# Kernel optimization log

Measured on AMD Instinct MI355X. Metric: run time of the kernel, lower is better.

The kernel has to match this reference:

```python
import jax, jax.numpy as jnp
import numpy as np

LRELU = 0.2
BN_EPS = 1e-5
SN_EPS = 1e-12


def _spectral_norm(w, u):
    # One power iteration (torch train-mode behavior), u/v detached.
    wm = w.reshape(w.shape[0], -1)            # [out, in*kh*kw]
    u = jax.lax.stop_gradient(u)
    v = wm.T @ u
    v = v / (jnp.linalg.norm(v) + SN_EPS)
    u2 = wm @ v
    u2 = u2 / (jnp.linalg.norm(u2) + SN_EPS)
    sigma = u2 @ (wm @ v)
    return w / sigma


def _conv(x, w):
    # Conv2d kernel=4, stride=2, padding=1, no bias
    return jax.lax.conv_general_dilated(
        x, w, window_strides=(2, 2), padding=((1, 1), (1, 1)),
        dimension_numbers=("NCHW", "OIHW", "NCHW"))


def _bn(x, g, b):
    # BatchNorm2d in training mode: biased batch stats over (N,H,W)
    m = x.mean(axis=(0, 2, 3), keepdims=True)
    v = x.var(axis=(0, 2, 3), keepdims=True)
    xh = (x - m) * jax.lax.rsqrt(v + BN_EPS)
    return xh * g[None, :, None, None] + b[None, :, None, None]


def _lrelu(x):
    return jnp.where(x >= 0, x, LRELU * x)


def setup_inputs() -> dict:
    key = jax.random.key(0)
    ks = jax.random.split(key, 16)
    ndf, nc, oc, N = 64, 3, 64, 64
    chans = [(nc, ndf), (ndf, ndf * 2), (ndf * 2, ndf * 4),
             (ndf * 4, ndf * 4), (ndf * 4, ndf * 8), (ndf * 8, oc)]
    inp = {"image": jax.random.normal(ks[0], (N, nc, 128, 128), jnp.float32)}
    for i, (ci, co) in enumerate(chans):
        inp[f"w{i+1}"] = 0.02 * jax.random.normal(ks[1 + i], (co, ci, 4, 4), jnp.float32)
        inp[f"u{i+1}"] = jax.random.normal(ks[7 + i], (co,), jnp.float32)
    for i, c in enumerate([ndf * 2, ndf * 4, ndf * 4, ndf * 8]):
        inp[f"g{i+1}"] = jnp.ones((c,), jnp.float32)
        inp[f"b{i+1}"] = jnp.zeros((c,), jnp.float32)
    A, B, C = oc * 2 * 2, oc, ndf  # 256, 64, 64
    stddev = 1.0 / A
    inp["T"] = jax.random.uniform(ks[13], (A, B, C), jnp.float32,
                                  minval=stddev, maxval=1.0)
    return inp


def reference(image, w1, w2, w3, w4, w5, w6, u1, u2, u3, u4, u5, u6,
              g1, b1, g2, b2, g3, b3, g4, b4, T):
    x = _lrelu(_conv(image, _spectral_norm(w1, u1)))
    x = _lrelu(_bn(_conv(x, _spectral_norm(w2, u2)), g1, b1))
    x = _lrelu(_bn(_conv(x, _spectral_norm(w3, u3)), g2, b2))
    x = _lrelu(_bn(_conv(x, _spectral_norm(w4, u4)), g3, b3))
    x = _lrelu(_bn(_conv(x, _spectral_norm(w5, u5)), g4, b4))
    x = _conv(x, _spectral_norm(w6, u6))          # [N, 64, 2, 2]; Dropout2d(p=0) = identity
    A, Bo, C = T.shape
    flat = x.reshape(-1, A)                        # [N, 256]
    Ms = (flat @ T.reshape(A, Bo * C)).reshape(-1, Bo, C)   # [N, B, C]
    # MiniBatchDiscrimination: out[i,b] = sum_j exp(-||Ms[i,b]-Ms[j,b]||_1)
    d = jnp.abs(Ms[:, None, :, :] - Ms[None, :, :, :]).sum(-1)  # [N, N, B]
    mbd = jnp.exp(-d).sum(axis=1)                  # [N, B]
    return jnp.concatenate([flat, mbd], axis=1)    # [N, 320]
```

## Files before the change

kernel.cpp:

```cpp
#include <hip/hip_runtime.h>
#include <hip/hip_bf16.h>
#include <math.h>

#define LRELU 0.2f
#define BN_EPS 1e-5f
#define SN_EPS 1e-12f

typedef __attribute__((ext_vector_type(4))) float f32x4;
typedef __attribute__((ext_vector_type(8))) short bf16x8;
typedef __attribute__((ext_vector_type(4))) short bf16x4;

__device__ inline float bf2f(short s) {
  union { unsigned u; float f; } c; c.u = ((unsigned)(unsigned short)s) << 16; return c.f;
}
__device__ inline short f2bf(float f) {
  __hip_bfloat16 h = __float2bfloat16(f); return *(short*)&h;
}

__device__ inline int xcd_swz(int bx, int nwg) {
  int chunk = nwg >> 3;
  return (bx & 7) * chunk + (bx >> 3);
}

__device__ inline float blockReduceSum256(float v, volatile float* red) {
  #pragma unroll
  for (int o = 32; o > 0; o >>= 1) v += __shfl_down(v, o, 64);
  const int tid = threadIdx.x;
  __syncthreads();
  if ((tid & 63) == 0) red[tid >> 6] = v;
  __syncthreads();
  return red[0] + red[1] + red[2] + red[3];
}

struct SNArgs {
  const float* w[6];
  const float* u[6];
  int outc[6];
  int ink[6];
};

__global__ __launch_bounds__(256) void sn_v(SNArgs args, float* __restrict__ vpart) {
  const int l = blockIdx.z;
  const int in_k = args.ink[l], out_c = args.outc[l];
  const int tid = threadIdx.x;
  const int j = blockIdx.x * 256 + tid;
  if (blockIdx.x * 256 >= in_k) return;
  const int rows = out_c >> 3;
  const int i0 = blockIdx.y * rows;
  __shared__ float uS[64];
  if (tid < rows) uS[tid] = args.u[l][i0 + tid];
  __syncthreads();
  if (j >= in_k) return;
  const float* __restrict__ w = args.w[l] + (size_t)i0 * in_k;
  float t = 0.f;
  for (int i = 0; i < rows; ++i) t = fmaf(w[(size_t)i * in_k + j], uS[i], t);
  vpart[((size_t)(l * 8 + blockIdx.y)) * 8192 + j] = t;
}

__global__ __launch_bounds__(256) void sn_v_red(SNArgs args, const float* __restrict__ vpart,
                                                float* __restrict__ vbuf, float* __restrict__ pA) {
  const int l = blockIdx.y;
  const int in_k = args.ink[l];
  const int tid = threadIdx.x;
  const int j = blockIdx.x * 256 + tid;
  __shared__ float red[4];
  float s = 0.f;
  if (j < in_k) {
    #pragma unroll
    for (int ch = 0; ch < 8; ++ch)
      s += vpart[((size_t)(l * 8 + ch)) * 8192 + j];
    vbuf[l * 8192 + j] = s;
  }
  const float bs = blockReduceSum256((j < in_k) ? s * s : 0.f, red);
  if (tid == 0) pA[l * 32 + blockIdx.x] = bs;
}

__global__ __launch_bounds__(64) void sn_norm1(SNArgs args, const float* __restrict__ pA,
                                               float* __restrict__ rinv) {
  const int l = blockIdx.x;
  if (threadIdx.x != 0) return;
  const int nb = (args.ink[l] + 255) >> 8;
  float s = 0.f;
  for (int b = 0; b < nb; ++b) s += pA[l * 32 + b];
  rinv[l] = 1.f / (sqrtf(s) + SN_EPS);
}

__global__ __launch_bounds__(256) void sn_t2(SNArgs args, const float* __restrict__ vbuf,
                                             const float* __restrict__ rinv,
                                             float* __restrict__ pB) {
  const int l = blockIdx.y;
  const int in_k = args.ink[l], out_c = args.outc[l];
  const int lane = threadIdx.x & 63, wv = threadIdx.x >> 6;
  const int row = blockIdx.x * 4 + wv;
  __shared__ float red[4];
  float sq = 0.f;
  if (row < out_c) {
    const float* __restrict__ wr = args.w[l] + (size_t)row * in_k;
    const float* __restrict__ v = vbuf + l * 8192;
    float a0 = 0.f, a1 = 0.f, a2 = 0.f, a3 = 0.f;
    for (int j = lane * 4; j < in_k; j += 256) {
      f32x4 w4 = *(const f32x4*)(wr + j);
      f32x4 v4 = *(const f32x4*)(v + j);
      a0 = fmaf(w4[0], v4[0], a0);
      a1 = fmaf(w4[1], v4[1], a1);
      a2 = fmaf(w4[2], v4[2], a2);
      a3 = fmaf(w4[3], v4[3], a3);
    }
    float t = (a0 + a1) + (a2 + a3);
    #pragma unroll
    for (int o = 32; o > 0; o >>= 1) t += __shfl_down(t, o, 64);
    if (lane == 0) { t *= rinv[l]; sq = t * t; }
  }
  __syncthreads();
  if (lane == 0) red[wv] = sq;
  __syncthreads();
  if (threadIdx.x == 0) pB[l * 128 + blockIdx.x] = red[0] + red[1] + red[2] + red[3];
}

__global__ __launch_bounds__(64) void sn_norm2(const float* __restrict__ pB,
                                               float* __restrict__ inv_sigma) {
  const int l = blockIdx.x;
  if (threadIdx.x != 0) return;
  float s = 0.f;
  for (int b = 0; b < 128; ++b) s += pB[l * 128 + b];
  const float n2 = sqrtf(s);
  const float sigma = s / (n2 + SN_EPS);
  inv_sigma[l] = 1.f / sigma;
}

__global__ __launch_bounds__(256) void zero_pads(__hip_bfloat16* r0, __hip_bfloat16* r1) {
  int t = blockIdx.x * 256 + threadIdx.x;
  if (t < 2048) {
    r0[16777216 + t] = __float2bfloat16(0.f);
    r1[16777216 + t] = __float2bfloat16(0.f);
  }
}

struct PPArgs {
  const float* w[6];
  __hip_bfloat16* dst[6];
  int cinr[6];
  int cout[6];
  int kpad[6];
  int kreal[6];
};

__global__ __launch_bounds__(256) void prepack_all(PPArgs args, const float* __restrict__ invs) {
  const int l = blockIdx.y;
  int e = blockIdx.x * 256 + threadIdx.x;
  const int total = args.kpad[l] * args.cout[l];
  if (e >= total) return;
  const int CINR = args.cinr[l], COUT = args.cout[l], KREAL = args.kreal[l];
  int j = e & 7, lane = (e >> 3) & 63, frag = e >> 9;
  int nfrags = COUT >> 4;
  int ks = frag / nfrags, nf = frag - ks * nfrags;
  int k = ks * 32 + ((lane >> 4) << 3) + j;
  int co = (nf << 4) + (lane & 15);
  float val = 0.f;
  if (k < KREAL) {
    int khw = k / CINR, ci = k - khw * CINR;
    int kh = khw >> 2, kw = khw & 3;
    val = args.w[l][(((size_t)co * CINR + ci) * 4 + kh) * 4 + kw] * invs[l];
  }
  args.dst[l][e] = __float2bfloat16(val);
}

__global__ __launch_bounds__(256) void im2col_l1(const float* __restrict__ img,
                                                 __hip_bfloat16* __restrict__ a2) {
  int t = blockIdx.x * 256 + threadIdx.x;
  int c = t & 7;
  int m = t >> 3;
  int n = m >> 12;
  int hw = m & 4095;
  int ho = hw >> 6, wo = hw & 63;
  int ihb = 2 * ho - 1, iwb = 2 * wo - 1;
  const float* __restrict__ ib = img + (size_t)n * 49152;
  short vals[8];
  #pragma unroll
  for (int j = 0; j < 8; ++j) {
    int k = c * 8 + j;
    float val = 0.f;
    if (k < 48) {
      int khw = k / 3;
      int ci = k - khw * 3;
      int kh = khw >> 2, kw = khw & 3;
      int ih = ihb + kh, iw = iwb + kw;
      if (((unsigned)ih < 128u) & ((unsigned)iw < 128u))
        val = ib[ci * 16384 + ih * 128 + iw];
    }
    vals[j] = f2bf(val);
  }
  *(bf16x8*)(a2 + (size_t)m * 64 + c * 8) = *(bf16x8*)vals;
}

template<int CIN, int COUT, int MF, bool FUSE>
__global__ __launch_bounds__(256) void conv_mfma(
    const __hip_bfloat16* __restrict__ x,
    const __hip_bfloat16* __restrict__ wf,
    __hip_bfloat16* __restrict__ out)
{
  constexpr int CB = CIN / 32;

  const int bx = xcd_swz(blockIdx.x, gridDim.x);
  const int lane = threadIdx.x & 63;
  const int wid  = threadIdx.x >> 6;
  const int wm = wid >> 1, wn = wid & 1;
  const int mbase = bx * (MF * 32) + wm * (MF * 16);
  const int cobase = blockIdx.y * 64 + wn * 32;

  int offm[MF];
  #pragma unroll
  for (int mf = 0; mf < MF; ++mf) {
    int m = mbase + mf * 16 + (lane & 15);
    offm[mf] = m * CIN;
  }
  const int koff = (lane >> 4) << 3;
  const __hip_bfloat16* wfp = wf + ((size_t)((blockIdx.y * 4 + wn * 2) * 64 + lane)) * 8;

  f32x4 acc[MF][2];
  #pragma unroll
  for (int mf = 0; mf < MF; ++mf) {
    acc[mf][0] = (f32x4){0.f, 0.f, 0.f, 0.f};
    acc[mf][1] = (f32x4){0.f, 0.f, 0.f, 0.f};
  }

  #pragma unroll
  for (int cb = 0; cb < CB; ++cb) {
    bf16x8 a[MF], b[2];
    #pragma unroll
    for (int mf = 0; mf < MF; ++mf) a[mf] = *(const bf16x8*)(x + offm[mf] + koff + cb * 32);
    #pragma unroll
    for (int nf = 0; nf < 2; ++nf)
      b[nf] = *(const bf16x8*)(wfp + (size_t)cb * (COUT * 32) + nf * 512);
    #pragma unroll
    for (int mf = 0; mf < MF; ++mf)
      #pragma unroll
      for (int nf = 0; nf < 2; ++nf)
        acc[mf][nf] = __builtin_amdgcn_mfma_f32_16x16x32_bf16(a[mf], b[nf], acc[mf][nf], 0, 0, 0);
  }

  const int r0 = (lane >> 4) * 4;
  const int cw = cobase + (lane & 15);
  #pragma unroll
  for (int mf = 0; mf < MF; ++mf)
    #pragma unroll
    for (int nf = 0; nf < 2; ++nf)
      #pragma unroll
      for (int r = 0; r < 4; ++r) {
        float v = acc[mf][nf][r];
        if (FUSE) v = (v >= 0.f) ? v : LRELU * v;
        int m = mbase + mf * 16 + r0 + r;
        out[(size_t)m * COUT + (cw + nf * 16)] = __float2bfloat16(v);
      }
}

template<int CIN, int COUT, int HIN, int HOUT, int Z, bool SPLITK>
__global__ __launch_bounds__(256) void conv_mfma4(
    const __hip_bfloat16* __restrict__ x,
    const __hip_bfloat16* __restrict__ wf,
    __hip_bfloat16* __restrict__ outb, float* __restrict__ outp)
{
  constexpr int WIN = HIN, WO = HOUT;
  constexpr int CB = CIN / 32;
  constexpr int KHW_PER = 16 / Z;
  constexpr int PADOFF = 16777216;
  constexpr int M = 64 * HOUT * WO;

  const int bx = xcd_swz(blockIdx.x, gridDim.x);
  const int lane = threadIdx.x & 63;
  const int wid  = threadIdx.x >> 6;
  const int wm = wid >> 1, wn = wid & 1;
  const int mbase = bx * 128 + wm * 64;
  const int nbase = blockIdx.y * 128 + wn * 64;
  const int khw0 = blockIdx.z * KHW_PER;

  int offm[4], ihb[4], iwb[4];
  #pragma unroll
  for (int mf = 0; mf < 4; ++mf) {
    int m = mbase + mf * 16 + (lane & 15);
    int n = m / (HOUT * WO);
    int hw = m - n * (HOUT * WO);
    int ho = hw / WO, wo = hw - ho * WO;
    ihb[mf] = 2 * ho - 1;
    iwb[mf] = 2 * wo - 1;
    offm[mf] = ((n * HIN + ihb[mf]) * WIN + iwb[mf]) * CIN;
  }
  const int koff = (lane >> 4) << 3;
  const __hip_bfloat16* wfp = wf + ((size_t)((nbase >> 4) * 64 + lane)) * 8;

  f32x4 acc[4][4];
  #pragma unroll
  for (int mf = 0; mf < 4; ++mf)
    #pragma unroll
    for (int nf = 0; nf < 4; ++nf) acc[mf][nf] = (f32x4){0.f, 0.f, 0.f, 0.f};

  #pragma unroll
  for (int ki = 0; ki < KHW_PER; ++ki) {
    const int khw = khw0 + ki;
    const int kh = khw >> 2, kw = khw & 3;
    const __hip_bfloat16* ap[4];
    #pragma unroll
    for (int mf = 0; mf < 4; ++mf) {
      int ih = ihb[mf] + kh, iw = iwb[mf] + kw;
      bool v = ((unsigned)ih < (unsigned)HIN) & ((unsigned)iw < (unsigned)WIN);
      int off = v ? (offm[mf] + (kh * WIN + kw) * CIN + koff) : (PADOFF + koff);
      ap[mf] = x + off;
    }
    #pragma unroll
    for (int cb = 0; cb < CB; ++cb) {
      const int ks = khw * CB + cb;
      bf16x8 a[4], b[4];
      #pragma unroll
      for (int mf = 0; mf < 4; ++mf) a[mf] = *(const bf16x8*)(ap[mf] + cb * 32);
      #pragma unroll
      for (int nf = 0; nf < 4; ++nf)
        b[nf] = *(const bf16x8*)(wfp + (size_t)ks * (COUT * 32) + nf * 512);
      #pragma unroll
      for (int mf = 0; mf < 4; ++mf)
        #pragma unroll
        for (int nf = 0; nf < 4; ++nf)
          acc[mf][nf] = __builtin_amdgcn_mfma_f32_16x16x32_bf16(a[mf], b[nf], acc[mf][nf], 0, 0, 0);
    }
  }

  const int r0 = (lane >> 4) * 4;
  const int cw = nbase + (lane & 15);
  #pragma unroll
  for (int mf = 0; mf < 4; ++mf)
    #pragma unroll
    for (int nf = 0; nf < 4; ++nf)
      #pragma unroll
      for (int r = 0; r < 4; ++r) {
        const int m = mbase + mf * 16 + r0 + r;
        const int co = cw + nf * 16;
        if (SPLITK) {
          outp[(size_t)blockIdx.z * M * COUT + (size_t)m * COUT + co] = acc[mf][nf][r];
        } else {
          outb[(size_t)m * COUT + co] = __float2bfloat16(acc[mf][nf][r]);
        }
      }
}

template<int Z, int MCHUNKS>
__global__ __launch_bounds__(256) void sk_bn_fuse(const float* __restrict__ part,
                                                  __hip_bfloat16* __restrict__ xo,
                                                  float* __restrict__ statp, int M, int C) {
  const int chunk = blockIdx.x;
  const int c0 = blockIdx.y * 64 + (threadIdx.x & 7) * 8;
  const int mrow = threadIdx.x >> 3;
  const int rows = M / MCHUNKS;
  const size_t MC = (size_t)M * C;
  float s[8], s2[8];
  #pragma unroll
  for (int j = 0; j < 8; ++j) { s[j] = 0.f; s2[j] = 0.f; }
  for (int mi = mrow; mi < rows; mi += 32) {
    const int m = chunk * rows + mi;
    const size_t base = (size_t)m * C + c0;
    f32x4 a = *(const f32x4*)(part + base);
    f32x4 b = *(const f32x4*)(part + base + 4);
    #pragma unroll
    for (int z = 1; z < Z; ++z) {
      a += *(const f32x4*)(part + (size_t)z * MC + base);
      b += *(const f32x4*)(part + (size_t)z * MC + base + 4);
    }
    bf16x8 o;
    #pragma unroll
    for (int j = 0; j < 4; ++j) {
      o[j] = f2bf(a[j]);
      o[4 + j] = f2bf(b[j]);
      s[j] += a[j];       s2[j] = fmaf(a[j], a[j], s2[j]);
      s[4+j] += b[j];     s2[4+j] = fmaf(b[j], b[j], s2[4+j]);
    }
    *(bf16x8*)(xo + base) = o;
  }
  __shared__ float ls[8][256], ls2[8][256];
  const int t = threadIdx.x;
  #pragma unroll
  for (int j = 0; j < 8; ++j) { ls[j][t] = s[j]; ls2[j][t] = s2[j]; }
  __syncthreads();
  #pragma unroll
  for (int off = 16; off >= 1; off >>= 1) {
    if (mrow < off) {
      #pragma unroll
      for (int j = 0; j < 8; ++j) {
        ls[j][t]  += ls[j][t + off * 8];
        ls2[j][t] += ls2[j][t + off * 8];
      }
    }
    __syncthreads();
  }
  if (t < 8) {
    #pragma unroll
    for (int j = 0; j < 8; ++j) {
      statp[(size_t)chunk * C + c0 + j] = ls[j][t];
      statp[(size_t)(MCHUNKS + chunk) * C + c0 + j] = ls2[j][t];
    }
  }
}

__global__ __launch_bounds__(256) void conv_l6_mfma(
    const __hip_bfloat16* __restrict__ x,
    const __hip_bfloat16* __restrict__ wf,
    float* __restrict__ x6, float* __restrict__ out)
{
  constexpr int CIN = 512, COUT = 64, HIN = 4;
  constexpr int CB = CIN / 32;
  constexpr int PADOFF = 16777216;

  const int lane = threadIdx.x & 63;
  const int wid  = threadIdx.x >> 6;
  const int wm = wid >> 1, wn = wid & 1;
  const int mbase = blockIdx.x * 32 + wm * 16;

  int m0 = mbase + (lane & 15);
  int n = m0 >> 2;
  int hw = m0 & 3;
  int ho = hw >> 1, wo = hw & 1;
  int ihb = 2 * ho - 1;
  int iwb = 2 * wo - 1;
  int offm = ((n * HIN + ihb) * HIN + iwb) * CIN;

  const int koff = (lane >> 4) << 3;
  const __hip_bfloat16* wfp = wf + ((size_t)((wn * 2) * 64 + lane)) * 8;

  f32x4 acc[2];
  acc[0] = (f32x4){0.f, 0.f, 0.f, 0.f};
  acc[1] = (f32x4){0.f, 0.f, 0.f, 0.f};

  #pragma unroll
  for (int khw = 0; khw < 16; ++khw) {
    const int kh = khw >> 2, kw = khw & 3;
    const int ih = ihb + kh, iw = iwb + kw;
    const bool v = ((unsigned)ih < (unsigned)HIN) & ((unsigned)iw < (unsigned)HIN);
    const int off = v ? (offm + (kh * HIN + kw) * CIN + koff) : (PADOFF + koff);
    const __hip_bfloat16* ap = x + off;
    #pragma unroll
    for (int cb = 0; cb < CB; ++cb) {
      const int ks = khw * CB + cb;
      bf16x8 a = *(const bf16x8*)(ap + cb * 32);
      bf16x8 b0 = *(const bf16x8*)(wfp + (size_t)ks * (COUT * 32));
      bf16x8 b1 = *(const bf16x8*)(wfp + (size_t)ks * (COUT * 32) + 512);
      acc[0] = __builtin_amdgcn_mfma_f32_16x16x32_bf16(a, b0, acc[0], 0, 0, 0);
      acc[1] = __builtin_amdgcn_mfma_f32_16x16x32_bf16(a, b1, acc[1], 0, 0, 0);
    }
  }

  const int r0 = (lane >> 4) * 4;
  const int cw = wn * 32 + (lane & 15);
  #pragma unroll
  for (int nf = 0; nf < 2; ++nf)
    #pragma unroll
    for (int r = 0; r < 4; ++r) {
      int m = mbase + r0 + r;
      int nn = m >> 2, p = m & 3;
      float v = acc[nf][r];
      x6[(size_t)nn * 256 + (cw + nf * 16) * 4 + p] = v;
      out[(size_t)nn * 320 + (cw + nf * 16) * 4 + p] = v;
    }
}

template<int MCHUNKS>
__global__ __launch_bounds__(256) void bn_stats_a(const __hip_bfloat16* __restrict__ x,
                                                  float* __restrict__ part, int M, int C) {
  const int chunk = blockIdx.x;
  const int c0 = blockIdx.y * 64 + (threadIdx.x & 7) * 8;
  const int mrow = threadIdx.x >> 3;
  const int rows = M / MCHUNKS;
  float s[8], s2[8];
  #pragma unroll
  for (int j = 0; j < 8; ++j) { s[j] = 0.f; s2[j] = 0.f; }
  for (int mi = mrow; mi < rows; mi += 32) {
    const int m = chunk * rows + mi;
    bf16x8 v = *(const bf16x8*)(x + (size_t)m * C + c0);
    #pragma unroll
    for (int j = 0; j < 8; ++j) {
      float f = bf2f(v[j]);
      s[j] += f;
      s2[j] = fmaf(f, f, s2[j]);
    }
  }
  __shared__ float ls[8][256], ls2[8][256];
  const int t = threadIdx.x;
  #pragma unroll
  for (int j = 0; j < 8; ++j) { ls[j][t] = s[j]; ls2[j][t] = s2[j]; }
  __syncthreads();
  #pragma unroll
  for (int off = 16; off >= 1; off >>= 1) {
    if (mrow < off) {
      #pragma unroll
      for (int j = 0; j < 8; ++j) {
        ls[j][t]  += ls[j][t + off * 8];
        ls2[j][t] += ls2[j][t + off * 8];
      }
    }
    __syncthreads();
  }
  if (t < 8) {
    #pragma unroll
    for (int j = 0; j < 8; ++j) {
      part[(size_t)chunk * C + c0 + j] = ls[j][t];
      part[(size_t)(MCHUNKS + chunk) * C + c0 + j] = ls2[j][t];
    }
  }
}

template<int MCHUNKS>
__global__ __launch_bounds__(64) void bn_stats_b(const float* __restrict__ part,
                                                 const float* __restrict__ g,
                                                 const float* __restrict__ b,
                                                 float* __restrict__ sb, int M, int C) {
  int c = blockIdx.x * 64 + threadIdx.x;
  float s = 0.f, s2 = 0.f;
  for (int ch = 0; ch < MCHUNKS; ++ch) {
    s  += part[(size_t)ch * C + c];
    s2 += part[(size_t)(MCHUNKS + ch) * C + c];
  }
  float invM = 1.f / (float)M;
  float mean = s * invM;
  float var = s2 * invM - mean * mean;
  float scale = g[c] * rsqrtf(var + BN_EPS);
  sb[c] = scale;
  sb[C + c] = b[c] - mean * scale;
}

__global__ __launch_bounds__(256) void bn_apply(__hip_bfloat16* __restrict__ x,
                                                const float* __restrict__ sb,
                                                int C, int nvec) {
  int idx = blockIdx.x * 256 + threadIdx.x;
  if (idx >= nvec) return;
  size_t e = (size_t)idx * 8;
  int c0 = (int)(e % (size_t)C);
  bf16x8 v = *(bf16x8*)(x + e);
  bf16x8 o;
  #pragma unroll
  for (int j = 0; j < 8; ++j) {
    int c = c0 + j;
    float f = bf2f(v[j]);
    f = fmaf(f, sb[c], sb[C + c]);
    f = (f >= 0.f) ? f : LRELU * f;
    o[j] = f2bf(f);
  }
  *(bf16x8*)(x + e) = o;
}

__global__ __launch_bounds__(256) void ms_kernel(const float* __restrict__ x6,
                                                 const float* __restrict__ T,
                                                 float* __restrict__ Ms) {
  const int cb = blockIdx.x;
  const int nb = blockIdx.y;
  const int c  = threadIdx.x & 63;
  const int ns = threadIdx.x >> 6;
  __shared__ float fsh[16][256];
  for (int t = threadIdx.x; t < 4096; t += 256) {
    int n = t >> 8, a = t & 255;
    fsh[n][a] = x6[(size_t)(nb * 16 + n) * 256 + a];
  }
  __syncthreads();
  const int col = cb * 64 + c;
  float acc0 = 0.f, acc1 = 0.f, acc2 = 0.f, acc3 = 0.f;
  #pragma unroll 8
  for (int a = 0; a < 256; ++a) {
    float tv = T[(size_t)a * 4096 + col];
    acc0 = fmaf(fsh[ns * 4 + 0][a], tv, acc0);
    acc1 = fmaf(fsh[ns * 4 + 1][a], tv, acc1);
    acc2 = fmaf(fsh[ns * 4 + 2][a], tv, acc2);
    acc3 = fmaf(fsh[ns * 4 + 3][a], tv, acc3);
  }
  const int nbase = nb * 16 + ns * 4;
  Ms[(size_t)(nbase + 0) * 4096 + col] = acc0;
  Ms[(size_t)(nbase + 1) * 4096 + col] = acc1;
  Ms[(size_t)(nbase + 2) * 4096 + col] = acc2;
  Ms[(size_t)(nbase + 3) * 4096 + col] = acc3;
}

__global__ __launch_bounds__(256) void mbd_kernel(const float* __restrict__ Ms,
                                                  float* __restrict__ out) {
  const int b  = blockIdx.x;
  const int ib = blockIdx.y;
  const int tid = threadIdx.x;
  __shared__ float Mb[64][65];
  for (int idx = tid; idx < 4096; idx += 256) {
    const int i = idx >> 6, cc = idx & 63;
    Mb[i][cc] = Ms[(size_t)i * 4096 + b * 64 + cc];
  }
  __syncthreads();
  const int i  = ib * 16 + (tid >> 4);
  const int jg = tid & 15;
  float ssum = 0.f;
  for (int j = jg; j < 64; j += 16) {
    float d = 0.f;
    #pragma unroll
    for (int cc = 0; cc < 64; ++cc) d += fabsf(Mb[i][cc] - Mb[j][cc]);
    ssum += expf(-d);
  }
  ssum += __shfl_xor(ssum, 1, 64);
  ssum += __shfl_xor(ssum, 2, 64);
  ssum += __shfl_xor(ssum, 4, 64);
  ssum += __shfl_xor(ssum, 8, 64);
  if (jg == 0) out[(size_t)i * 320 + 256 + b] = ssum;
}

extern "C" void kernel_launch(void* const* d_in, const int* in_sizes, int n_in,
                              void* d_out, int out_size, void* d_ws, size_t ws_size,
                              hipStream_t stream) {
  const float* image = (const float*)d_in[0];
  const float* W[6] = {(const float*)d_in[1], (const float*)d_in[3], (const float*)d_in[5],
                       (const float*)d_in[7], (const float*)d_in[9], (const float*)d_in[11]};
  const float* U[6] = {(const float*)d_in[2], (const float*)d_in[4], (const float*)d_in[6],
                       (const float*)d_in[8], (const float*)d_in[10], (const float*)d_in[12]};
  const float* G[4] = {(const float*)d_in[13], (const float*)d_in[15],
                       (const float*)d_in[17], (const float*)d_in[19]};
  const float* Bb[4] = {(const float*)d_in[14], (const float*)d_in[16],
                        (const float*)d_in[18], (const float*)d_in[20]};
  const float* T = (const float*)d_in[21];
  float* out = (float*)d_out;

  float* f = (float*)d_ws;
  float* inv_sigma = f;
  float* part      = f + 1024;
  float* sb        = f + 1024 + 65536;
  float* x6        = f + 1024 + 65536 + 1024;
  float* Ms        = f + 1024 + 65536 + 1024 + 16384;
  float* vbuf      = f + 360448;
  float* pA        = f + 360448 + 49152;
  float* pB        = pA + 256;
  float* rinv      = pB + 768;
  __hip_bfloat16* bfb = (__hip_bfloat16*)(f + 524288);
  const size_t REGION = 16777216 + 2048;
  __hip_bfloat16* region0 = bfb;
  __hip_bfloat16* region1 = region0 + REGION;
  __hip_bfloat16* wf1 = region1 + REGION;
  __hip_bfloat16* wf2 = wf1 + 4096;
  __hip_bfloat16* wf3 = wf2 + 131072;
  __hip_bfloat16* wf4 = wf3 + 524288;
  __hip_bfloat16* wf5 = wf4 + 1048576;
  __hip_bfloat16* wf6 = wf5 + 2097152;
  float* skpart = (float*)(wf6 + 524288);
  float* vpart  = skpart + 8388608;

  __hip_bfloat16* a2col = region0;
  __hip_bfloat16* x1 = region1;
  __hip_bfloat16* x2 = region0;
  __hip_bfloat16* x3 = region1;
  __hip_bfloat16* x4 = region0;
  __hip_bfloat16* x5 = region1;

  zero_pads<<<8, 256, 0, stream>>>(region0, region1);

  SNArgs sa;
  const int outc[6] = {64, 128, 256, 256, 512, 64};
  const int ink[6]  = {48, 1024, 2048, 4096, 4096, 8192};
  for (int l = 0; l < 6; ++l) { sa.w[l] = W[l]; sa.u[l] = U[l]; sa.outc[l] = outc[l]; sa.ink[l] = ink[l]; }

  sn_v<<<dim3(32, 8, 6), 256, 0, stream>>>(sa, vpart);
  sn_v_red<<<dim3(32, 6), 256, 0, stream>>>(sa, vpart, vbuf, pA);
  sn_norm1<<<6, 64, 0, stream>>>(sa, pA, rinv);
  sn_t2<<<dim3(128, 6), 256, 0, stream>>>(sa, vbuf, rinv, pB);
  sn_norm2<<<6, 64, 0, stream>>>(pB, inv_sigma);

  PPArgs pa;
  __hip_bfloat16* wfp_[6] = {wf1, wf2, wf3, wf4, wf5, wf6};
  const int cinr_[6]  = {3, 64, 128, 256, 256, 512};
  const int kpad_[6]  = {64, 1024, 2048, 4096, 4096, 8192};
  const int kreal_[6] = {48, 1024, 2048, 4096, 4096, 8192};
  for (int l = 0; l < 6; ++l) {
    pa.w[l] = W[l]; pa.dst[l] = wfp_[l]; pa.cinr[l] = cinr_[l];
    pa.cout[l] = outc[l]; pa.kpad[l] = kpad_[l]; pa.kreal[l] = kreal_[l];
  }
  prepack_all<<<dim3(8192, 6), 256, 0, stream>>>(pa, inv_sigma);

  im2col_l1<<<8192, 256, 0, stream>>>(image, a2col);

  conv_mfma<64, 64, 4, true><<<dim3(2048, 1), 256, 0, stream>>>(a2col, wf1, x1);

  conv_mfma4<64, 128, 64, 32, 1, false><<<dim3(512, 1, 1), 256, 0, stream>>>(x1, wf2, x2, nullptr);
  bn_stats_a<256><<<dim3(256, 2), 256, 0, stream>>>(x2, part, 65536, 128);
  bn_stats_b<256><<<2, 64, 0, stream>>>(part, G[0], Bb[0], sb, 65536, 128);
  bn_apply<<<4096, 256, 0, stream>>>(x2, sb, 128, 1048576);

  conv_mfma4<128, 256, 32, 16, 2, true><<<dim3(128, 2, 2), 256, 0, stream>>>(x2, wf3, nullptr, skpart);
  sk_bn_fuse<2, 128><<<dim3(128, 4), 256, 0, stream>>>(skpart, x3, part, 16384, 256);
  bn_stats_b<128><<<4, 64, 0, stream>>>(part, G[1], Bb[1], sb, 16384, 256);
  bn_apply<<<2048, 256, 0, stream>>>(x3, sb, 256, 524288);

  conv_mfma4<256, 256, 16, 8, 8, true><<<dim3(32, 2, 8), 256, 0, stream>>>(x3, wf4, nullptr, skpart);
  sk_bn_fuse<8, 128><<<dim3(128, 4), 256, 0, stream>>>(skpart, x4, part, 4096, 256);
  bn_stats_b<128><<<4, 64, 0, stream>>>(part, G[2], Bb[2], sb, 4096, 256);
  bn_apply<<<512, 256, 0, stream>>>(x4, sb, 256, 131072);

  conv_mfma4<256, 512, 8, 4, 16, true><<<dim3(8, 4, 16), 256, 0, stream>>>(x4, wf5, nullptr, skpart);
  sk_bn_fuse<16, 32><<<dim3(32, 8), 256, 0, stream>>>(skpart, x5, part, 1024, 512);
  bn_stats_b<32><<<8, 64, 0, stream>>>(part, G[3], Bb[3], sb, 1024, 512);
  bn_apply<<<256, 256, 0, stream>>>(x5, sb, 512, 65536);

  conv_l6_mfma<<<8, 256, 0, stream>>>(x5, wf6, x6, out);

  ms_kernel<<<dim3(64, 4), 256, 0, stream>>>(x6, T, Ms);
  mbd_kernel<<<dim3(64, 4), 256, 0, stream>>>(Ms, out);
}
```

Baseline: 375.6 us.

## Fuse BatchNorm apply and LeakyReLU into next conv's input loads

Removes the four standalone bn_apply passes and instead applies the per-channel scale/shift and LeakyReLU to activation fragments as they are loaded in the following convolution, including the final layer-6 conv. The loop order is swapped so channel-block scale/shift vectors are loaded once per cb and reused across kernel taps, and padded taps are forced to zero after the transform. This saves a read-modify-write pass over each intermediate activation and four launches. In exchange, each input element is re-normalized once per overlapping tap (up to about four times), which adds ALU work inside the MFMA loop.

```diff
diff --git a/kernel.cpp b/kernel.cpp
--- a/kernel.cpp
+++ b/kernel.cpp
@@ -254,10 +254,11 @@
       }
 }
 
-template<int CIN, int COUT, int HIN, int HOUT, int Z, bool SPLITK>
+template<int CIN, int COUT, int HIN, int HOUT, int Z, bool SPLITK, bool BNIN>
 __global__ __launch_bounds__(256) void conv_mfma4(
     const __hip_bfloat16* __restrict__ x,
     const __hip_bfloat16* __restrict__ wf,
+    const float* __restrict__ sbp,
     __hip_bfloat16* __restrict__ outb, float* __restrict__ outp)
 {
   constexpr int WIN = HIN, WO = HOUT;
@@ -295,26 +296,49 @@
     for (int nf = 0; nf < 4; ++nf) acc[mf][nf] = (f32x4){0.f, 0.f, 0.f, 0.f};
 
   #pragma unroll
-  for (int ki = 0; ki < KHW_PER; ++ki) {
-    const int khw = khw0 + ki;
-    const int kh = khw >> 2, kw = khw & 3;
-    const __hip_bfloat16* ap[4];
-    #pragma unroll
-    for (int mf = 0; mf < 4; ++mf) {
-      int ih = ihb[mf] + kh, iw = iwb[mf] + kw;
-      bool v = ((unsigned)ih < (unsigned)HIN) & ((unsigned)iw < (unsigned)WIN);
-      int off = v ? (offm[mf] + (kh * WIN + kw) * CIN + koff) : (PADOFF + koff);
-      ap[mf] = x + off;
-    }
-    #pragma unroll
-    for (int cb = 0; cb < CB; ++cb) {
-      const int ks = khw * CB + cb;
+  for (int cb = 0; cb < CB; ++cb) {
+    f32x4 s0, s1, o0, o1;
+    if (BNIN) {
+      const int cbase = cb * 32 + koff;
+      s0 = *(const f32x4*)(sbp + cbase);
+      s1 = *(const f32x4*)(sbp + cbase + 4);
+      o0 = *(const f32x4*)(sbp + CIN + cbase);
+      o1 = *(const f32x4*)(sbp + CIN + cbase + 4);
+    }
+    #pragma unroll
+    for (int ki = 0; ki < KHW_PER; ++ki) {
+      const int khw = khw0 + ki;
+      const int kh = khw >> 2, kw = khw & 3;
       bf16x8 a[4], b[4];
-      #pragma unroll
-      for (int mf = 0; mf < 4; ++mf) a[mf] = *(const bf16x8*)(ap[mf] + cb * 32);
+      bool vm[4];
+      #pragma unroll
+      for (int mf = 0; mf < 4; ++mf) {
+        int ih = ihb[mf] + kh, iw = iwb[mf] + kw;
+        vm[mf] = ((unsigned)ih < (unsigned)HIN) & ((unsigned)iw < (unsigned)WIN);
+        int off = vm[mf] ? (offm[mf] + (kh * WIN + kw) * CIN + koff + cb * 32)
+                         : (PADOFF + koff + cb * 32);
+        a[mf] = *(const bf16x8*)(x + off);
+      }
+      const size_t ks = (size_t)khw * CB + cb;
       #pragma unroll
       for (int nf = 0; nf < 4; ++nf)
-        b[nf] = *(const bf16x8*)(wfp + (size_t)ks * (COUT * 32) + nf * 512);
+        b[nf] = *(const bf16x8*)(wfp + ks * (COUT * 32) + nf * 512);
+      if (BNIN) {
+        #pragma unroll
+        for (int mf = 0; mf < 4; ++mf) {
+          bf16x8 t = a[mf];
+          #pragma unroll
+          for (int j = 0; j < 8; ++j) {
+            float fv = bf2f(t[j]);
+            float sc = (j < 4) ? s0[j] : s1[j - 4];
+            float of = (j < 4) ? o0[j] : o1[j - 4];
+            fv = fmaf(fv, sc, of);
+            fv = (fv >= 0.f) ? fv : LRELU * fv;
+            t[j] = vm[mf] ? f2bf(fv) : (short)0;
+          }
+          a[mf] = t;
+        }
+      }
       #pragma unroll
       for (int mf = 0; mf < 4; ++mf)
         #pragma unroll
@@ -401,6 +425,7 @@
 __global__ __launch_bounds__(256) void conv_l6_mfma(
     const __hip_bfloat16* __restrict__ x,
     const __hip_bfloat16* __restrict__ wf,
+    const float* __restrict__ sbp,
     float* __restrict__ x6, float* __restrict__ out)
 {
   constexpr int CIN = 512, COUT = 64, HIN = 4;
@@ -428,18 +453,32 @@
   acc[1] = (f32x4){0.f, 0.f, 0.f, 0.f};
 
   #pragma unroll
-  for (int khw = 0; khw < 16; ++khw) {
-    const int kh = khw >> 2, kw = khw & 3;
-    const int ih = ihb + kh, iw = iwb + kw;
-    const bool v = ((unsigned)ih < (unsigned)HIN) & ((unsigned)iw < (unsigned)HIN);
-    const int off = v ? (offm + (kh * HIN + kw) * CIN + koff) : (PADOFF + koff);
-    const __hip_bfloat16* ap = x + off;
-    #pragma unroll
-    for (int cb = 0; cb < CB; ++cb) {
-      const int ks = khw * CB + cb;
-      bf16x8 a = *(const bf16x8*)(ap + cb * 32);
-      bf16x8 b0 = *(const bf16x8*)(wfp + (size_t)ks * (COUT * 32));
-      bf16x8 b1 = *(const bf16x8*)(wfp + (size_t)ks * (COUT * 32) + 512);
+  for (int cb = 0; cb < CB; ++cb) {
+    const int cbase = cb * 32 + koff;
+    f32x4 s0 = *(const f32x4*)(sbp + cbase);
+    f32x4 s1 = *(const f32x4*)(sbp + cbase + 4);
+    f32x4 o0 = *(const f32x4*)(sbp + CIN + cbase);
+    f32x4 o1 = *(const f32x4*)(sbp + CIN + cbase + 4);
+    #pragma unroll
+    for (int khw = 0; khw < 16; ++khw) {
+      const int kh = khw >> 2, kw = khw & 3;
+      const int ih = ihb + kh, iw = iwb + kw;
+      const bool v = ((unsigned)ih < (unsigned)HIN) & ((unsigned)iw < (unsigned)HIN);
+      const int off = v ? (offm + (kh * HIN + kw) * CIN + koff + cb * 32)
+                        : (PADOFF + koff + cb * 32);
+      bf16x8 a = *(const bf16x8*)(x + off);
+      #pragma unroll
+      for (int j = 0; j < 8; ++j) {
+        float fv = bf2f(a[j]);
+        float sc = (j < 4) ? s0[j] : s1[j - 4];
+        float of = (j < 4) ? o0[j] : o1[j - 4];
+        fv = fmaf(fv, sc, of);
+        fv = (fv >= 0.f) ? fv : LRELU * fv;
+        a[j] = v ? f2bf(fv) : (short)0;
+      }
+      const size_t ks = (size_t)khw * CB + cb;
+      bf16x8 b0 = *(const bf16x8*)(wfp + ks * (COUT * 32));
+      bf16x8 b1 = *(const bf16x8*)(wfp + ks * (COUT * 32) + 512);
       acc[0] = __builtin_amdgcn_mfma_f32_16x16x32_bf16(a, b0, acc[0], 0, 0, 0);
       acc[1] = __builtin_amdgcn_mfma_f32_16x16x32_bf16(a, b1, acc[1], 0, 0, 0);
     }
@@ -521,26 +560,6 @@
   float scale = g[c] * rsqrtf(var + BN_EPS);
   sb[c] = scale;
   sb[C + c] = b[c] - mean * scale;
-}
-
-__global__ __launch_bounds__(256) void bn_apply(__hip_bfloat16* __restrict__ x,
-                                                const float* __restrict__ sb,
-                                                int C, int nvec) {
-  int idx = blockIdx.x * 256 + threadIdx.x;
-  if (idx >= nvec) return;
-  size_t e = (size_t)idx * 8;
-  int c0 = (int)(e % (size_t)C);
-  bf16x8 v = *(bf16x8*)(x + e);
-  bf16x8 o;
-  #pragma unroll
-  for (int j = 0; j < 8; ++j) {
-    int c = c0 + j;
-    float f = bf2f(v[j]);
-    f = fmaf(f, sb[c], sb[C + c]);
-    f = (f >= 0.f) ? f : LRELU * f;
-    o[j] = f2bf(f);
-  }
-  *(bf16x8*)(x + e) = o;
 }
 
 __global__ __launch_bounds__(256) void ms_kernel(const float* __restrict__ x6,
@@ -618,13 +637,14 @@
   float* f = (float*)d_ws;
   float* inv_sigma = f;
   float* part      = f + 1024;
-  float* sb        = f + 1024 + 65536;
   float* x6        = f + 1024 + 65536 + 1024;
   float* Ms        = f + 1024 + 65536 + 1024 + 16384;
   float* vbuf      = f + 360448;
   float* pA        = f + 360448 + 49152;
   float* pB        = pA + 256;
   float* rinv      = pB + 768;
+  float* sbL[4];
+  for (int i = 0; i < 4; ++i) sbL[i] = f + 412672 + i * 2048;
   __hip_bfloat16* bfb = (__hip_bfloat16*)(f + 524288);
   const size_t REGION = 16777216 + 2048;
   __hip_bfloat16* region0 = bfb;
@@ -673,27 +693,23 @@
 
   conv_mfma<64, 64, 4, true><<<dim3(2048, 1), 256, 0, stream>>>(a2col, wf1, x1);
 
-  conv_mfma4<64, 128, 64, 32, 1, false><<<dim3(512, 1, 1), 256, 0, stream>>>(x1, wf2, x2, nullptr);
+  conv_mfma4<64, 128, 64, 32, 1, false, false><<<dim3(512, 1, 1), 256, 0, stream>>>(x1, wf2, nullptr, x2, nullptr);
   bn_stats_a<256><<<dim3(256, 2), 256, 0, stream>>>(x2, part, 65536, 128);
-  bn_stats_b<256><<<2, 64, 0, stream>>>(part, G[0], Bb[0], sb, 65536, 128);
-  bn_apply<<<4096, 256, 0, stream>>>(x2, sb, 128, 1048576);
-
-  conv_mfma4<128, 256, 32, 16, 2, true><<<dim3(128, 2, 2), 256, 0, stream>>>(x2, wf3, nullptr, skpart);
+  bn_stats_b<256><<<2, 64, 0, stream>>>(part, G[0], Bb[0], sbL[0], 65536, 128);
+
+  conv_mfma4<128, 256, 32, 16, 2, true, true><<<dim3(128, 2, 2), 256, 0, stream>>>(x2, wf3, sbL[0], nullptr, skpart);
   sk_bn_fuse<2, 128><<<dim3(128, 4), 256, 0, stream>>>(skpart, x3, part, 16384, 256);
-  bn_stats_b<128><<<4, 64, 0, stream>>>(part, G[1], Bb[1], sb, 16384, 256);
-  bn_apply<<<2048, 256, 0, stream>>>(x3, sb, 256, 524288);
-
-  conv_mfma4<256, 256, 16, 8, 8, true><<<dim3(32, 2, 8), 256, 0, stream>>>(x3, wf4, nullptr, skpart);
+  bn_stats_b<128><<<4, 64, 0, stream>>>(part, G[1], Bb[1], sbL[1], 16384, 256);
+
+  conv_mfma4<256, 256, 16, 8, 8, true, true><<<dim3(32, 2, 8), 256, 0, stream>>>(x3, wf4, sbL[1], nullptr, skpart);
   sk_bn_fuse<8, 128><<<dim3(128, 4), 256, 0, stream>>>(skpart, x4, part, 4096, 256);
-  bn_stats_b<128><<<4, 64, 0, stream>>>(part, G[2], Bb[2], sb, 4096, 256);
-  bn_apply<<<512, 256, 0, stream>>>(x4, sb, 256, 131072);
-
-  conv_mfma4<256, 512, 8, 4, 16, true><<<dim3(8, 4, 16), 256, 0, stream>>>(x4, wf5, nullptr, skpart);
+  bn_stats_b<128><<<4, 64, 0, stream>>>(part, G[2], Bb[2], sbL[2], 4096, 256);
+
+  conv_mfma4<256, 512, 8, 4, 16, true, true><<<dim3(8, 4, 16), 256, 0, stream>>>(x4, wf5, sbL[2], nullptr, skpart);
   sk_bn_fuse<16, 32><<<dim3(32, 8), 256, 0, stream>>>(skpart, x5, part, 1024, 512);
-  bn_stats_b<32><<<8, 64, 0, stream>>>(part, G[3], Bb[3], sb, 1024, 512);
-  bn_apply<<<256, 256, 0, stream>>>(x5, sb, 512, 65536);
-
-  conv_l6_mfma<<<8, 256, 0, stream>>>(x5, wf6, x6, out);
+  bn_stats_b<32><<<8, 64, 0, stream>>>(part, G[3], Bb[3], sbL[3], 1024, 512);
+
+  conv_l6_mfma<<<8, 256, 0, stream>>>(x5, wf6, sbL[3], x6, out);
 
   ms_kernel<<<dim3(64, 4), 256, 0, stream>>>(x6, T, Ms);
   mbd_kernel<<<dim3(64, 4), 256, 0, stream>>>(Ms, out);
```

After: 439.4 us. +17.0%, slower.
